# Optimization experiments

Hardware: AMD Instinct MI355X
Metric: run time of the kernel (lower is better)

The kernel has to match this reference:

```python
import jax, jax.numpy as jnp
import numpy as np

B, S, I, H = 64, 256, 1024, 1024


def setup_inputs() -> dict:
    key = jax.random.key(0)
    stdv = 1.0 / np.sqrt(H)
    inp = {}
    key, kx = jax.random.split(key)
    inp["x"] = jax.random.normal(kx, (B, S, I), jnp.float32)
    names = ["W_f", "Wm_f", "W_i", "Wm_i", "W_o", "Wm_o", "W_c", "Wm_c",
             "U_f", "Um_f", "U_i", "Um_i", "U_o", "Um_o", "U_c", "Um_c",
             "b_f", "b_i", "b_o", "b_c"]
    for n in names:
        key, sub = jax.random.split(key)
        if n.startswith("W"):
            shape = (H, I)
        elif n.startswith("U"):
            shape = (H, H)
        else:
            shape = (H,)
        inp[n] = jax.random.uniform(sub, shape, jnp.float32, -stdv, stdv)
    return inp


def _mlin(x, W, Wm):
    # MaskedLinear, wise='feat': sigmoid(x @ Wm^T) * (x @ W^T)
    return jax.nn.sigmoid(x @ Wm.T) * (x @ W.T)


def reference(x, W_f, Wm_f, W_i, Wm_i, W_o, Wm_o, W_c, Wm_c,
              U_f, Um_f, U_i, Um_i, U_o, Um_o, U_c, Um_c,
              b_f, b_i, b_o, b_c):
    # input-side masked linears depend only on x: hoist out of the recurrence
    xf = jnp.moveaxis(_mlin(x, W_f, Wm_f), 1, 0)  # (S,B,H)
    xi = jnp.moveaxis(_mlin(x, W_i, Wm_i), 1, 0)
    xo = jnp.moveaxis(_mlin(x, W_o, Wm_o), 1, 0)
    xc = jnp.moveaxis(_mlin(x, W_c, Wm_c), 1, 0)

    def step(carry, g):
        h, c = carry
        gf, gi, go, gc = g
        f = jax.nn.sigmoid(gf + _mlin(h, U_f, Um_f) + b_f)
        i = jax.nn.sigmoid(gi + _mlin(h, U_i, Um_i) + b_i)
        o = jax.nn.sigmoid(go + _mlin(h, U_o, Um_o) + b_o)
        c = jnp.tanh(gc + _mlin(h, U_c, Um_c) + b_c) * i + f * c
        h = o * c
        return (h, c), h

    h0 = jnp.zeros((B, H), x.dtype)
    (h, c), out = jax.lax.scan(step, (h0, h0), (xf, xi, xo, xc))
    output = jnp.moveaxis(out, 0, 1)  # (B,S,H)
    return output, h[None], c[None]  # h,c: (1,B,H)
```

## Files before the change

### kernel.cpp

```cpp
#include <hip/hip_runtime.h>

typedef float f32x4 __attribute__((ext_vector_type(4)));
typedef _Float16 f16x8 __attribute__((ext_vector_type(8)));
typedef _Float16 f16x4 __attribute__((ext_vector_type(4)));

typedef const __attribute__((address_space(1))) unsigned int* gptr_t;
typedef __attribute__((address_space(3))) unsigned int* lptr_t;

__device__ __forceinline__ unsigned short f2h_u(float f){
  union { _Float16 h; unsigned short u; } cv; cv.h = (_Float16)f; return cv.u;
}
__device__ __forceinline__ float h2f(unsigned short u){
  union { unsigned short u; _Float16 h; } cv; cv.u = u; return (float)cv.h;
}
__device__ __forceinline__ float sigmoidf_(float x){ return 1.0f / (1.0f + __expf(-x)); }

#define LOADC2(dst, c)                                                         \
  _Pragma("unroll")                                                            \
  for (int i = 0; i < 8; ++i){                                                 \
    const int p0 = pbase + (c) * 16 + (i & 1) * 8;                             \
    const int ro = ((i >> 1) * 16 + r) * 4;                                    \
    f16x4 lo_ = *(const f16x4*)(hb2 + (size_t)p0 * 256 + ro);                  \
    f16x4 hi_ = *(const f16x4*)(hb2 + (size_t)(p0 + 1) * 256 + ro);            \
    dst[i] = __builtin_shufflevector(lo_, hi_, 0, 1, 2, 3, 4, 5, 6, 7);        \
  }

#define COMPC(buf, c)                                                          \
  _Pragma("unroll")                                                            \
  for (int kk = 0; kk < 2; ++kk)                                               \
    _Pragma("unroll")                                                          \
    for (int nt = 0; nt < 2; ++nt)                                             \
      _Pragma("unroll")                                                        \
      for (int mt = 0; mt < 4; ++mt)                                           \
        acc[nt][mt] = __builtin_amdgcn_mfma_f32_16x16x32_f16(                  \
            uf[nt][(c) * 2 + kk], buf[mt * 2 + kk], acc[nt][mt], 0, 0, 0);

__global__ __launch_bounds__(256) void cvt_x(const float* __restrict__ in,
                                             unsigned short* __restrict__ out){
  int idx = blockIdx.x * 256 + threadIdx.x;
  int d4 = idx * 4;
  int s = d4 >> 16, b = (d4 >> 10) & 63, k = d4 & 1023;
  const float4 v = *(const float4*)(in + (size_t)b * 262144 + (size_t)s * 1024 + k);
  ushort4 o;
  o.x = f2h_u(v.x); o.y = f2h_u(v.y); o.z = f2h_u(v.z); o.w = f2h_u(v.w);
  *(ushort4*)(out + d4) = o;
}

struct P8 { const float* p[8]; };

__global__ __launch_bounds__(256) void cvt_w8(P8 mats, unsigned short* __restrict__ out){
  int idx = blockIdx.x * 256 + threadIdx.x;
  int e = idx * 4;
  int mi = e >> 20, off = e & 1048575;
  const float4 v = *(const float4*)(mats.p[mi] + off);
  ushort4 o;
  o.x = f2h_u(v.x); o.y = f2h_u(v.y); o.z = f2h_u(v.z); o.w = f2h_u(v.w);
  *(ushort4*)(out + e) = o;
}

__global__ __launch_bounds__(256) void pack8(P8 mats, unsigned short* __restrict__ out){
  int idx = blockIdx.x * 256 + threadIdx.x;
  int e = idx * 4;
  int j = e >> 10, k = e & 1023;
  int m = j & 7, row = j >> 3;
  const float4 v = *(const float4*)(mats.p[m] + (size_t)row * 1024 + k);
  ushort4 o;
  o.x = f2h_u(v.x); o.y = f2h_u(v.y); o.z = f2h_u(v.z); o.w = f2h_u(v.w);
  *(ushort4*)(out + e) = o;
}

__global__ __launch_bounds__(256, 2) void gemmz(
    const unsigned short* __restrict__ Xh,
    const unsigned short* __restrict__ Wg,
    unsigned short* __restrict__ Z01,
    unsigned short* __restrict__ Z23){
  __shared__ unsigned short As[128 * 32];
  __shared__ unsigned short Bl[128 * 32];
  __shared__ unsigned short Bm[128 * 32];
  const int tid = threadIdx.x;
  const int wave = tid >> 6, lane = tid & 63;
  const int r = lane & 15, q = lane >> 4;
  const int bid0 = blockIdx.x;
  const int bid = (bid0 & 7) * 512 + (bid0 >> 3);
  const int m0 = (bid & 127) * 128;
  const int n0 = ((bid >> 7) & 7) * 128;
  const int g  = bid >> 10;
  const int wm = wave >> 1, wn = wave & 1;

  const unsigned short* WL = Wg + ((size_t)(2 * g) << 20);
  const unsigned short* WM = WL + (1u << 20);

  f32x4 accL[4][4], accM[4][4];
#pragma unroll
  for (int a = 0; a < 4; ++a)
#pragma unroll
    for (int b = 0; b < 4; ++b){ accL[a][b] = 0.f; accM[a][b] = 0.f; }

  const int st_rl = lane >> 2;
  const int st_s0 = lane & 3;

  for (int kt = 0; kt < 32; ++kt){
    const int k0 = kt * 32;
#pragma unroll
    for (int j = 0; j < 2; ++j){
      const int c = wave * 2 + j;
      const int row = c * 16 + st_rl;
      const int slot = st_s0 ^ ((row >> 1) & 3);
      const unsigned short* sA = Xh + (size_t)(m0 + row) * 1024 + k0 + slot * 8;
      const unsigned short* sL = WL + (size_t)(n0 + row) * 1024 + k0 + slot * 8;
      const unsigned short* sM = WM + (size_t)(n0 + row) * 1024 + k0 + slot * 8;
      __builtin_amdgcn_global_load_lds((gptr_t)sA, (lptr_t)(As + c * 512), 16, 0, 0);
      __builtin_amdgcn_global_load_lds((gptr_t)sL, (lptr_t)(Bl + c * 512), 16, 0, 0);
      __builtin_amdgcn_global_load_lds((gptr_t)sM, (lptr_t)(Bm + c * 512), 16, 0, 0);
    }
    __syncthreads();

    f16x8 af[4], bl[4], bm[4];
#pragma unroll
    for (int mt = 0; mt < 4; ++mt){
      const int row = wm * 64 + mt * 16 + r;
      const int slot = q ^ ((row >> 1) & 3);
      af[mt] = *(const f16x8*)(As + row * 32 + slot * 8);
    }
#pragma unroll
    for (int nt = 0; nt < 4; ++nt){
      const int row = wn * 64 + nt * 16 + r;
      const int slot = q ^ ((row >> 1) & 3);
      bl[nt] = *(const f16x8*)(Bl + row * 32 + slot * 8);
      bm[nt] = *(const f16x8*)(Bm + row * 32 + slot * 8);
    }
#pragma unroll
    for (int nt = 0; nt < 4; ++nt)
#pragma unroll
      for (int mt = 0; mt < 4; ++mt){
        accL[mt][nt] = __builtin_amdgcn_mfma_f32_16x16x32_f16(af[mt], bl[nt], accL[mt][nt], 0, 0, 0);
        accM[mt][nt] = __builtin_amdgcn_mfma_f32_16x16x32_f16(af[mt], bm[nt], accM[mt][nt], 0, 0, 0);
      }
    __syncthreads();
  }

  unsigned short* Zp = (g < 2) ? (Z01 + ((size_t)g << 24)) : (Z23 + ((size_t)(g - 2) << 24));
#pragma unroll
  for (int mt = 0; mt < 4; ++mt)
#pragma unroll
    for (int nt = 0; nt < 4; ++nt){
      f32x4 aL = accL[mt][nt], aM = accM[mt][nt];
      union { ushort4 u; uint2 d; } o;
      o.u.x = f2h_u(aL[0] * sigmoidf_(aM[0]));
      o.u.y = f2h_u(aL[1] * sigmoidf_(aM[1]));
      o.u.z = f2h_u(aL[2] * sigmoidf_(aM[2]));
      o.u.w = f2h_u(aL[3] * sigmoidf_(aM[3]));
      const int gn = n0 + wn * 64 + nt * 16 + r;
      const int gm = m0 + wm * 64 + mt * 16 + q * 4;
      *(uint2*)(Zp + (size_t)gn * 16384 + gm) = o.d;
    }
}

__global__ __launch_bounds__(256, 1) void lstm_rec(
    const unsigned short* __restrict__ zF, const unsigned short* __restrict__ zI,
    const unsigned short* __restrict__ zO, const unsigned short* __restrict__ zC,
    const unsigned short* __restrict__ Ug,
    const float* __restrict__ bF, const float* __restrict__ bI,
    const float* __restrict__ bO, const float* __restrict__ bC,
    unsigned short* __restrict__ hh2,
    unsigned int* __restrict__ flags,
    float* __restrict__ out){
  const int tid = threadIdx.x, wave = tid >> 6, lane = tid & 63;
  const int bi = blockIdx.x, n0 = bi * 4, j0 = bi * 32;
  const int r = lane & 15, q = lane >> 4;
  const int pbase = wave * 64 + 2 * q;
  __shared__ __align__(16) float part[4][64][36];

  const unsigned int* f0 = flags + (size_t)lane * 32;
  const unsigned int* f1 = flags + (size_t)(lane + 64) * 32;
  const unsigned int* f2 = flags + (size_t)(lane + 128) * 32;
  const unsigned int* f3 = flags + (size_t)(lane + 192) * 32;

  f16x8 uf[2][8];
#pragma unroll
  for (int nt = 0; nt < 2; ++nt)
#pragma unroll
    for (int kk = 0; kk < 8; ++kk)
      uf[nt][kk] = *(const f16x8*)(Ug + (size_t)(j0 + nt * 16 + r) * 1024 + wave * 256 + kk * 32 + q * 8);

  const int cb = tid >> 2, cl = tid & 3;
  const float bFv = bF[n0 + cl], bIv = bI[n0 + cl], bOv = bO[n0 + cl], bCv = bC[n0 + cl];
  const size_t zb = (size_t)(n0 + cl) * 16384 + cb;
  float c_reg = 0.f;

#pragma unroll 1
  for (int s = 0; s < 256; ++s){
    float zf = h2f(zF[zb + s * 64]);
    float zi = h2f(zI[zb + s * 64]);
    float zo = h2f(zO[zb + s * 64]);
    float zc = h2f(zC[zb + s * 64]);

    f32x4 acc[2][4];
#pragma unroll
    for (int nt = 0; nt < 2; ++nt)
#pragma unroll
      for (int mt = 0; mt < 4; ++mt) acc[nt][mt] = 0.f;

    if (s > 0){
      const unsigned tgt = (unsigned)s;
      if (wave == 0){
        for (;;){
          unsigned a, b, c, d;
          asm volatile("global_load_dword %0, %1, off sc0 sc1" : "=v"(a) : "v"(f0) : "memory");
          asm volatile("global_load_dword %0, %1, off sc0 sc1" : "=v"(b) : "v"(f1) : "memory");
          asm volatile("global_load_dword %0, %1, off sc0 sc1" : "=v"(c) : "v"(f2) : "memory");
          asm volatile("global_load_dword %0, %1, off sc0 sc1" : "=v"(d) : "v"(f3) : "memory");
          asm volatile("s_waitcnt vmcnt(0)" ::: "memory");
          int ok = (a >= tgt) & (b >= tgt) & (c >= tgt) & (d >= tgt);
          if (__all(ok)) break;
        }
      }
      __syncthreads();

      const unsigned short* hb2 = hh2 + (size_t)(s - 1) * 65536;
      f16x8 hA[8], hB[8];
      LOADC2(hA, 0);
      LOADC2(hB, 1);
      COMPC(hA, 0);
      LOADC2(hA, 2);
      COMPC(hB, 1);
      LOADC2(hB, 3);
      COMPC(hA, 2);
      COMPC(hB, 3);
    }

#pragma unroll
    for (int nt = 0; nt < 2; ++nt)
#pragma unroll
      for (int mt = 0; mt < 4; ++mt)
        *(f32x4*)&part[wave][mt * 16 + r][nt * 16 + q * 4] = acc[nt][mt];
    __syncthreads();

    f32x4 y0 = 0.f, y1 = 0.f;
#pragma unroll
    for (int w = 0; w < 4; ++w){
      y0 += *(const f32x4*)&part[w][cb][cl * 8];
      y1 += *(const f32x4*)&part[w][cb][cl * 8 + 4];
    }

    float fg = sigmoidf_(zf + y0[0] * sigmoidf_(y0[1]) + bFv);
    float ig = sigmoidf_(zi + y0[2] * sigmoidf_(y0[3]) + bIv);
    float og = sigmoidf_(zo + y1[0] * sigmoidf_(y1[1]) + bOv);
    float cg = tanhf   (zc + y1[2] * sigmoidf_(y1[3]) + bCv);
    c_reg = cg * ig + fg * c_reg;
    float h = og * c_reg;

    float hn = __shfl_xor(h, 1);
    if (!(cl & 1)){
      unsigned int pv = (unsigned)f2h_u(h) | ((unsigned)f2h_u(hn) << 16);
      const unsigned short* hw = hh2 + (size_t)s * 65536 + bi * 256 + cb * 4 + cl;
      asm volatile("global_store_dword %0, %1, off sc0 sc1" :: "v"(hw), "v"(pv) : "memory");
    }
    if (s == 255){
      out[16777216 + cb * 1024 + n0 + cl] = h;
      out[16777216 + 65536 + cb * 1024 + n0 + cl] = c_reg;
      break;
    }
    asm volatile("s_waitcnt vmcnt(0)" ::: "memory");
    __syncthreads();
    if (tid == 0){
      unsigned int v = (unsigned)(s + 1);
      const unsigned int* fw = flags + (size_t)bi * 32;
      asm volatile("global_store_dword %0, %1, off sc0 sc1" :: "v"(fw), "v"(v) : "memory");
    }
  }
}

__global__ __launch_bounds__(256) void expand_out(const unsigned short* __restrict__ hh2,
                                                  float* __restrict__ out){
  int idx = blockIdx.x * 256 + threadIdx.x;
  int p = idx & 255, s = (idx >> 8) & 255, cb = idx >> 16;
  f16x4 v = *(const f16x4*)(hh2 + (size_t)s * 65536 + p * 256 + cb * 4);
  float4 f = { (float)v[0], (float)v[1], (float)v[2], (float)v[3] };
  *(float4*)(out + ((size_t)cb * 256 + s) * 1024 + p * 4) = f;
}

extern "C" void kernel_launch(void* const* d_in, const int* in_sizes, int n_in,
                              void* d_out, int out_size, void* d_ws, size_t ws_size,
                              hipStream_t stream){
  (void)in_sizes; (void)n_in; (void)out_size; (void)ws_size;
  char* ws = (char*)d_ws;
  const float* bF = (const float*)d_in[17];
  const float* bI = (const float*)d_in[18];
  const float* bO = (const float*)d_in[19];
  const float* bC = (const float*)d_in[20];
  float* outp = (float*)d_out;
  P8 w8, u8;
  for (int m = 0; m < 8; ++m){
    w8.p[m] = (const float*)d_in[1 + m];
    u8.p[m] = (const float*)d_in[9 + m];
  }

  unsigned short* xh  = (unsigned short*)(ws);
  unsigned short* wg  = (unsigned short*)(ws + 33554432);
  unsigned short* ug  = (unsigned short*)(ws + 50331648);
  unsigned short* z23 = (unsigned short*)(ws + 67108864);
  unsigned short* hh2 = (unsigned short*)(ws + 134217728);
  unsigned int* flags = (unsigned int*)  (ws + 167772160);
  unsigned short* z01 = (unsigned short*)d_out;

  (void)hipMemsetAsync(flags, 0, 32768, stream);
  cvt_x<<<16384, 256, 0, stream>>>((const float*)d_in[0], xh);
  cvt_w8<<<8192, 256, 0, stream>>>(w8, wg);
  pack8<<<8192, 256, 0, stream>>>(u8, ug);
  gemmz<<<4096, 256, 0, stream>>>(xh, wg, z01, z23);

  const unsigned short* zF = z01;
  const unsigned short* zI = z01 + 16777216;
  const unsigned short* zO = z23;
  const unsigned short* zC = z23 + 16777216;

  void* args[] = { (void*)&zF, (void*)&zI, (void*)&zO, (void*)&zC, (void*)&ug,
                   (void*)&bF, (void*)&bI, (void*)&bO, (void*)&bC,
                   (void*)&hh2, (void*)&flags, (void*)&outp };
  if (hipLaunchCooperativeKernel((const void*)lstm_rec, dim3(256), dim3(256), args, 0u, stream) != hipSuccess)
    lstm_rec<<<256, 256, 0, stream>>>(zF, zI, zO, zC, ug, bF, bI, bO, bC, hh2, flags, outp);

  expand_out<<<16384, 256, 0, stream>>>(hh2, outp);
}
```

Before: 1.495 ms.

## Replace per-step flag barrier with sentinel-valued data polling on h buffer

```diff
diff --git a/kernel.cpp b/kernel.cpp
--- a/kernel.cpp
+++ b/kernel.cpp
@@ -3,6 +3,7 @@
 typedef float f32x4 __attribute__((ext_vector_type(4)));
 typedef _Float16 f16x8 __attribute__((ext_vector_type(8)));
 typedef _Float16 f16x4 __attribute__((ext_vector_type(4)));
+typedef unsigned int u32x2 __attribute__((ext_vector_type(2)));
 
 typedef const __attribute__((address_space(1))) unsigned int* gptr_t;
 typedef __attribute__((address_space(3))) unsigned int* lptr_t;
@@ -14,26 +15,48 @@
   union { unsigned short u; _Float16 h; } cv; cv.u = u; return (float)cv.h;
 }
 __device__ __forceinline__ float sigmoidf_(float x){ return 1.0f / (1.0f + __expf(-x)); }
-
-#define LOADC2(dst, c)                                                         \
+__device__ __forceinline__ unsigned umax_(unsigned a, unsigned b){ return a > b ? a : b; }
+
+#define ISSUEC(LO, HI, c)                                                      \
   _Pragma("unroll")                                                            \
   for (int i = 0; i < 8; ++i){                                                 \
     const int p0 = pbase + (c) * 16 + (i & 1) * 8;                             \
     const int ro = ((i >> 1) * 16 + r) * 4;                                    \
-    f16x4 lo_ = *(const f16x4*)(hb2 + (size_t)p0 * 256 + ro);                  \
-    f16x4 hi_ = *(const f16x4*)(hb2 + (size_t)(p0 + 1) * 256 + ro);            \
-    dst[i] = __builtin_shufflevector(lo_, hi_, 0, 1, 2, 3, 4, 5, 6, 7);        \
-  }
-
-#define COMPC(buf, c)                                                          \
+    const unsigned short* alo_ = hb2 + (size_t)p0 * 256 + ro;                  \
+    const unsigned short* ahi_ = hb2 + (size_t)(p0 + 1) * 256 + ro;            \
+    asm volatile("global_load_dwordx2 %0, %1, off sc0 sc1"                     \
+                 : "=v"(LO[i]) : "v"(alo_) : "memory");                        \
+    asm volatile("global_load_dwordx2 %0, %1, off sc0 sc1"                     \
+                 : "=v"(HI[i]) : "v"(ahi_) : "memory");                        \
+  }
+
+#define WAITVALC(LO, HI, c)                                                    \
+  for (;;){                                                                    \
+    asm volatile("s_waitcnt vmcnt(0)" ::: "memory");                           \
+    __builtin_amdgcn_sched_barrier(0);                                         \
+    unsigned mx_ = 0;                                                          \
+    _Pragma("unroll")                                                          \
+    for (int i = 0; i < 8; ++i)                                                \
+      mx_ = umax_(mx_, umax_(umax_(LO[i][0], LO[i][1]),                        \
+                             umax_(HI[i][0], HI[i][1])));                      \
+    if (__all(mx_ != 0xFFFFFFFFu)) break;                                      \
+    ISSUEC(LO, HI, c);                                                         \
+  }
+
+#define COMPC2(LO, HI, c)                                                      \
   _Pragma("unroll")                                                            \
   for (int kk = 0; kk < 2; ++kk)                                               \
     _Pragma("unroll")                                                          \
     for (int nt = 0; nt < 2; ++nt)                                             \
       _Pragma("unroll")                                                        \
-      for (int mt = 0; mt < 4; ++mt)                                           \
+      for (int mt = 0; mt < 4; ++mt){                                          \
+        const int i_ = mt * 2 + kk;                                            \
+        f16x8 hf_ = __builtin_shufflevector(*(const f16x4*)&LO[i_],            \
+                                            *(const f16x4*)&HI[i_],            \
+                                            0, 1, 2, 3, 4, 5, 6, 7);           \
         acc[nt][mt] = __builtin_amdgcn_mfma_f32_16x16x32_f16(                  \
-            uf[nt][(c) * 2 + kk], buf[mt * 2 + kk], acc[nt][mt], 0, 0, 0);
+            uf[nt][(c) * 2 + kk], hf_, acc[nt][mt], 0, 0, 0);                  \
+      }
 
 __global__ __launch_bounds__(256) void cvt_x(const float* __restrict__ in,
                                              unsigned short* __restrict__ out){
@@ -163,18 +186,12 @@
     const float* __restrict__ bF, const float* __restrict__ bI,
     const float* __restrict__ bO, const float* __restrict__ bC,
     unsigned short* __restrict__ hh2,
-    unsigned int* __restrict__ flags,
     float* __restrict__ out){
   const int tid = threadIdx.x, wave = tid >> 6, lane = tid & 63;
   const int bi = blockIdx.x, n0 = bi * 4, j0 = bi * 32;
   const int r = lane & 15, q = lane >> 4;
   const int pbase = wave * 64 + 2 * q;
-  __shared__ __align__(16) float part[4][64][36];
-
-  const unsigned int* f0 = flags + (size_t)lane * 32;
-  const unsigned int* f1 = flags + (size_t)(lane + 64) * 32;
-  const unsigned int* f2 = flags + (size_t)(lane + 128) * 32;
-  const unsigned int* f3 = flags + (size_t)(lane + 192) * 32;
+  __shared__ __align__(16) float part[2][4][64][36];
 
   f16x8 uf[2][8];
 #pragma unroll
@@ -202,45 +219,35 @@
       for (int mt = 0; mt < 4; ++mt) acc[nt][mt] = 0.f;
 
     if (s > 0){
-      const unsigned tgt = (unsigned)s;
-      if (wave == 0){
-        for (;;){
-          unsigned a, b, c, d;
-          asm volatile("global_load_dword %0, %1, off sc0 sc1" : "=v"(a) : "v"(f0) : "memory");
-          asm volatile("global_load_dword %0, %1, off sc0 sc1" : "=v"(b) : "v"(f1) : "memory");
-          asm volatile("global_load_dword %0, %1, off sc0 sc1" : "=v"(c) : "v"(f2) : "memory");
-          asm volatile("global_load_dword %0, %1, off sc0 sc1" : "=v"(d) : "v"(f3) : "memory");
-          asm volatile("s_waitcnt vmcnt(0)" ::: "memory");
-          int ok = (a >= tgt) & (b >= tgt) & (c >= tgt) & (d >= tgt);
-          if (__all(ok)) break;
-        }
-      }
-      __syncthreads();
-
       const unsigned short* hb2 = hh2 + (size_t)(s - 1) * 65536;
-      f16x8 hA[8], hB[8];
-      LOADC2(hA, 0);
-      LOADC2(hB, 1);
-      COMPC(hA, 0);
-      LOADC2(hA, 2);
-      COMPC(hB, 1);
-      LOADC2(hB, 3);
-      COMPC(hA, 2);
-      COMPC(hB, 3);
-    }
-
+      u32x2 Alo[8], Ahi[8], Blo[8], Bhi[8];
+      ISSUEC(Alo, Ahi, 0);
+      WAITVALC(Alo, Ahi, 0);
+      ISSUEC(Blo, Bhi, 1);
+      COMPC2(Alo, Ahi, 0);
+      WAITVALC(Blo, Bhi, 1);
+      ISSUEC(Alo, Ahi, 2);
+      COMPC2(Blo, Bhi, 1);
+      WAITVALC(Alo, Ahi, 2);
+      ISSUEC(Blo, Bhi, 3);
+      COMPC2(Alo, Ahi, 2);
+      WAITVALC(Blo, Bhi, 3);
+      COMPC2(Blo, Bhi, 3);
+    }
+
+    const int pp = s & 1;
 #pragma unroll
     for (int nt = 0; nt < 2; ++nt)
 #pragma unroll
       for (int mt = 0; mt < 4; ++mt)
-        *(f32x4*)&part[wave][mt * 16 + r][nt * 16 + q * 4] = acc[nt][mt];
+        *(f32x4*)&part[pp][wave][mt * 16 + r][nt * 16 + q * 4] = acc[nt][mt];
     __syncthreads();
 
     f32x4 y0 = 0.f, y1 = 0.f;
 #pragma unroll
     for (int w = 0; w < 4; ++w){
-      y0 += *(const f32x4*)&part[w][cb][cl * 8];
-      y1 += *(const f32x4*)&part[w][cb][cl * 8 + 4];
+      y0 += *(const f32x4*)&part[pp][w][cb][cl * 8];
+      y1 += *(const f32x4*)&part[pp][w][cb][cl * 8 + 4];
     }
 
     float fg = sigmoidf_(zf + y0[0] * sigmoidf_(y0[1]) + bFv);
@@ -259,14 +266,6 @@
     if (s == 255){
       out[16777216 + cb * 1024 + n0 + cl] = h;
       out[16777216 + 65536 + cb * 1024 + n0 + cl] = c_reg;
-      break;
-    }
-    asm volatile("s_waitcnt vmcnt(0)" ::: "memory");
-    __syncthreads();
-    if (tid == 0){
-      unsigned int v = (unsigned)(s + 1);
-      const unsigned int* fw = flags + (size_t)bi * 32;
-      asm volatile("global_store_dword %0, %1, off sc0 sc1" :: "v"(fw), "v"(v) : "memory");
     }
   }
 }
@@ -301,10 +300,9 @@
   unsigned short* ug  = (unsigned short*)(ws + 50331648);
   unsigned short* z23 = (unsigned short*)(ws + 67108864);
   unsigned short* hh2 = (unsigned short*)(ws + 134217728);
-  unsigned int* flags = (unsigned int*)  (ws + 167772160);
   unsigned short* z01 = (unsigned short*)d_out;
 
-  (void)hipMemsetAsync(flags, 0, 32768, stream);
+  (void)hipMemsetAsync(hh2, 0xFF, 33554432, stream);
   cvt_x<<<16384, 256, 0, stream>>>((const float*)d_in[0], xh);
   cvt_w8<<<8192, 256, 0, stream>>>(w8, wg);
   pack8<<<8192, 256, 0, stream>>>(u8, ug);
@@ -317,9 +315,9 @@
 
   void* args[] = { (void*)&zF, (void*)&zI, (void*)&zO, (void*)&zC, (void*)&ug,
                    (void*)&bF, (void*)&bI, (void*)&bO, (void*)&bC,
-                   (void*)&hh2, (void*)&flags, (void*)&outp };
+                   (void*)&hh2, (void*)&outp };
   if (hipLaunchCooperativeKernel((const void*)lstm_rec, dim3(256), dim3(256), args, 0u, stream) != hipSuccess)
-    lstm_rec<<<256, 256, 0, stream>>>(zF, zI, zO, zC, ug, bF, bI, bO, bC, hh2, flags, outp);
+    lstm_rec<<<256, 256, 0, stream>>>(zF, zI, zO, zC, ug, bF, bI, bO, bC, hh2, outp);
 
   expand_out<<<16384, 256, 0, stream>>>(hh2, outp);
 }
```

Measured after the change: 1.455 ms. 1.03x faster.
